# Optimization experiments

Measured on AMD Instinct MI355X. Metric: run time of the kernel, lower is better.

Reference implementation:

```python
import jax, jax.numpy as jnp
import numpy as np

N_NODES = 100000
N_EDGES = 1600000
NFEAT = 512
HIDDEN = 128
NCLASS = 40


def setup_inputs() -> dict:
    key = jax.random.key(0)
    ks = jax.random.split(key, 8)
    x = jax.random.normal(ks[0], (N_NODES, NFEAT), dtype=jnp.float32)
    edge_src = jax.random.randint(ks[1], (N_EDGES,), 0, N_NODES, dtype=jnp.int32)
    edge_dst = jax.random.randint(ks[2], (N_EDGES,), 0, N_NODES, dtype=jnp.int32)
    # normalized adjacency values (D^-1/2 A D^-1/2 style), all positive
    edge_val = jax.random.uniform(ks[3], (N_EDGES,), dtype=jnp.float32)
    # glorot-ish init like pygcn's reset_parameters
    W1 = jax.random.normal(ks[4], (NFEAT, HIDDEN), dtype=jnp.float32) / np.sqrt(NFEAT)
    b1 = jnp.zeros((HIDDEN,), dtype=jnp.float32)
    W2 = jax.random.normal(ks[5], (HIDDEN, NCLASS), dtype=jnp.float32) / np.sqrt(HIDDEN)
    b2 = jnp.zeros((NCLASS,), dtype=jnp.float32)
    return {"x": x, "edge_src": edge_src, "edge_dst": edge_dst, "edge_val": edge_val,
            "W1": W1, "b1": b1, "W2": W2, "b2": b2}


def _gcn_layer(h, edge_src, edge_dst, edge_val, W, b):
    # support = h @ W ; out = spmm(adj, support) + b
    support = h @ W                                  # [N, d_out]
    msg = support[edge_src] * edge_val[:, None]      # [E, d_out] gather
    agg = jax.ops.segment_sum(msg, edge_dst, num_segments=N_NODES)  # scatter-add
    return agg + b


def reference(x, edge_src, edge_dst, edge_val, W1, b1, W2, b2):
    h = _gcn_layer(x, edge_src, edge_dst, edge_val, W1, b1)
    h = jax.nn.relu(h)
    # dropout=0.0 -> branch skipped (faithful to `if self.dropout:` with falsy value)
    h = _gcn_layer(h, edge_src, edge_dst, edge_val, W2, b2)
    return jax.nn.log_softmax(h, axis=1)
```

## Files before the change

kernel.cpp:

```cpp
#include <hip/hip_runtime.h>
#include <stdint.h>

#define NN 100000
#define NE 1600000
#define NF 512
#define NH 128
#define NC 40
#define DEGS 16
#define NGB 782
#define EPB 2048

typedef float f32x4 __attribute__((ext_vector_type(4)));
typedef short bf16x8 __attribute__((ext_vector_type(8)));

__device__ __forceinline__ unsigned short f2bf(float f){
    unsigned u = __float_as_uint(f);
    u = u + 0x7FFFu + ((u >> 16) & 1u);
    return (unsigned short)(u >> 16);
}
__device__ __forceinline__ unsigned pk2(float a, float b){
    return (unsigned)f2bf(a) | ((unsigned)f2bf(b) << 16);
}
__device__ __forceinline__ float blo(unsigned u){ return __uint_as_float(u << 16); }
__device__ __forceinline__ float bhi(unsigned u){ return __uint_as_float(u & 0xffff0000u); }
__device__ __forceinline__ float pval(unsigned p){ return __uint_as_float((p & 0x7fffu) << 16); }
__device__ __forceinline__ unsigned psrc(unsigned p){ return p >> 15; }

__global__ __launch_bounds__(256) void wprep(const float* __restrict__ W1, const float* __restrict__ W2,
                                             unsigned short* __restrict__ W1t, unsigned short* __restrict__ W2t){
    int tid = blockIdx.x * 256 + threadIdx.x;
    if (tid < NF * NH){
        int c = tid >> 9;
        int k = tid & 511;
        W1t[c * NF + k] = f2bf(W1[k * NH + c]);
    }
    int t2 = tid - NF * NH;
    if (t2 >= 0 && t2 < 48 * NH){
        int c = t2 >> 7;
        int k = t2 & 127;
        W2t[c * NH + k] = (c < NC) ? f2bf(W2[k * NC + c]) : (unsigned short)0;
    }
}

__global__ __launch_bounds__(256, 3) void gemm1_edge(const float* __restrict__ x,
                                                     const unsigned short* __restrict__ W1t,
                                                     unsigned short* __restrict__ s1,
                                                     const int* __restrict__ esrc,
                                                     const int* __restrict__ edst,
                                                     const float* __restrict__ eval,
                                                     unsigned* __restrict__ deg,
                                                     unsigned* __restrict__ pkc){
    __shared__ unsigned short Al[2][128 * 40];
    __shared__ unsigned short Bl[2][128 * 40];
    const int tid  = threadIdx.x;

    unsigned epv[8]; unsigned epos[8]; int edd[8];
    {
        const int ebase = blockIdx.x * EPB + tid;
#pragma unroll
        for (int i = 0; i < 8; i++){
            int e = ebase + i * 256;
            bool ok = e < NE;
            int d      = ok ? edst[e] : 0;
            int sv     = ok ? esrc[e] : 0;
            float ev   = ok ? eval[e] : 0.f;
            edd[i] = d;
            epv[i] = ((unsigned)sv << 15) | ((unsigned)f2bf(ev) & 0x7fffu);
            epos[i] = ok ? atomicAdd(&deg[d * DEGS], 1u) : 64u;
        }
    }

    const int wid  = tid >> 6;
    const int lane = tid & 63;
    const int quad = lane >> 4;
    const int l15  = lane & 15;
    const int br   = blockIdx.x * 128;

    const int r    = tid >> 1;
    const int half = tid & 1;

    int arow = br + r; if (arow >= NN) arow = NN - 1;
    const float* aptr = x + (size_t)arow * NF + half * 16;
    const unsigned short* bptr = W1t + (size_t)r * NF + half * 16;

    float4 pa0, pa1, pa2, pa3;
    uint4  pb0, pb1;
    {
        const float4* ap = (const float4*)aptr;
        pa0 = ap[0]; pa1 = ap[1]; pa2 = ap[2]; pa3 = ap[3];
        const uint4* bp = (const uint4*)bptr;
        pb0 = bp[0]; pb1 = bp[1];
        unsigned* Ad = (unsigned*)&Al[0][r * 40 + half * 16];
        Ad[0] = pk2(pa0.x, pa0.y); Ad[1] = pk2(pa0.z, pa0.w);
        Ad[2] = pk2(pa1.x, pa1.y); Ad[3] = pk2(pa1.z, pa1.w);
        Ad[4] = pk2(pa2.x, pa2.y); Ad[5] = pk2(pa2.z, pa2.w);
        Ad[6] = pk2(pa3.x, pa3.y); Ad[7] = pk2(pa3.z, pa3.w);
        uint4* Bd = (uint4*)&Bl[0][r * 40 + half * 16];
        Bd[0] = pb0; Bd[1] = pb1;
    }
    __syncthreads();

    f32x4 acc[2][8];
#pragma unroll
    for (int i = 0; i < 2; i++)
#pragma unroll
        for (int j = 0; j < 8; j++) acc[i][j] = (f32x4){0.f, 0.f, 0.f, 0.f};

    int cur = 0;
    for (int ks = 0; ks < NF; ks += 32){
        const bool more = (ks + 32 < NF);
        if (more){
            const float4* ap = (const float4*)(aptr + ks + 32);
            pa0 = ap[0]; pa1 = ap[1]; pa2 = ap[2]; pa3 = ap[3];
            const uint4* bp = (const uint4*)(bptr + ks + 32);
            pb0 = bp[0]; pb1 = bp[1];
        }

        bf16x8 a0 = *(const bf16x8*)&Al[cur][(wid * 32 +      l15) * 40 + quad * 8];
        bf16x8 a1 = *(const bf16x8*)&Al[cur][(wid * 32 + 16 + l15) * 40 + quad * 8];
        bf16x8 bb[8];
#pragma unroll
        for (int ct = 0; ct < 8; ct++)
            bb[ct] = *(const bf16x8*)&Bl[cur][(ct * 16 + l15) * 40 + quad * 8];
#pragma unroll
        for (int ct = 0; ct < 8; ct++){
            acc[0][ct] = __builtin_amdgcn_mfma_f32_16x16x32_bf16(a0, bb[ct], acc[0][ct], 0, 0, 0);
            acc[1][ct] = __builtin_amdgcn_mfma_f32_16x16x32_bf16(a1, bb[ct], acc[1][ct], 0, 0, 0);
        }

        if (more){
            int nxt = cur ^ 1;
            unsigned* Ad = (unsigned*)&Al[nxt][r * 40 + half * 16];
            Ad[0] = pk2(pa0.x, pa0.y); Ad[1] = pk2(pa0.z, pa0.w);
            Ad[2] = pk2(pa1.x, pa1.y); Ad[3] = pk2(pa1.z, pa1.w);
            Ad[4] = pk2(pa2.x, pa2.y); Ad[5] = pk2(pa2.z, pa2.w);
            Ad[6] = pk2(pa3.x, pa3.y); Ad[7] = pk2(pa3.z, pa3.w);
            uint4* Bd = (uint4*)&Bl[nxt][r * 40 + half * 16];
            Bd[0] = pb0; Bd[1] = pb1;
        }
        __syncthreads();
        cur ^= 1;
    }

#pragma unroll
    for (int rt = 0; rt < 2; rt++)
#pragma unroll
        for (int ct = 0; ct < 8; ct++)
#pragma unroll
            for (int i = 0; i < 4; i++){
                int row = br + wid * 32 + rt * 16 + quad * 4 + i;
                if (row < NN) s1[(size_t)row * NH + ct * 16 + l15] = f2bf(acc[rt][ct][i]);
            }

#pragma unroll
    for (int i = 0; i < 8; i++){
        if (epos[i] < 64u)
            pkc[(size_t)edd[i] * 64 + epos[i]] = epv[i];
    }
}

__global__ __launch_bounds__(256) void agg1g2(const uint4* __restrict__ s1v,
                                              const unsigned* __restrict__ deg,
                                              const unsigned* __restrict__ pkc,
                                              const float* __restrict__ b1,
                                              const unsigned short* __restrict__ W2t,
                                              unsigned short* __restrict__ s2p){
    __shared__ unsigned short Hl[64][136];
    const int tid   = threadIdx.x;
    const int wid   = tid >> 6;
    const int lane  = tid & 63;
    const int quad  = lane >> 4;
    const int hl    = lane & 15;
    const int lbase = quad * 16;
    const int nb    = blockIdx.x * 64;

    const float4* b1v = (const float4*)b1;
    const float4 bA = b1v[2 * hl], bB = b1v[2 * hl + 1];

#pragma unroll
    for (int pass = 0; pass < 4; pass++){
        const int nloc = pass * 16 + wid * 4 + quad;
        const int node = nb + nloc;
        float a[8];
#pragma unroll
        for (int t = 0; t < 8; t++) a[t] = 0.f;

        if (node < NN){
            const unsigned s = (unsigned)node * 64;
            unsigned dgv = deg[node * DEGS]; int dg = (dgv > 64u) ? 64 : (int)dgv;
            const unsigned e = s + dg;

            unsigned rec = 0;
            { int c0 = dg > 16 ? 16 : dg; if (hl < c0) rec = pkc[s + hl]; }
            for (unsigned base = s; base < e; base += 16){
                int cnt = (int)(e - base); if (cnt > 16) cnt = 16;
                unsigned curc = rec;
                unsigned nxb = base + 16;
                if (nxb < e){
                    int cn = (int)(e - nxb); if (cn > 16) cn = 16;
                    rec = 0;
                    if (hl < cn) rec = pkc[nxb + hl];
                }
                int j = 0;
                for (; j + 8 <= cnt; j += 8){
                    unsigned ps[8];
#pragma unroll
                    for (int q = 0; q < 8; q++) ps[q] = __shfl(curc, lbase + j + q, 64);
                    uint4 us[8];
#pragma unroll
                    for (int q = 0; q < 8; q++) us[q] = s1v[(size_t)psrc(ps[q]) * 16 + hl];
#pragma unroll
                    for (int q = 0; q < 8; q++){
                        float v = pval(ps[q]);
                        a[0] += v * blo(us[q].x); a[1] += v * bhi(us[q].x);
                        a[2] += v * blo(us[q].y); a[3] += v * bhi(us[q].y);
                        a[4] += v * blo(us[q].z); a[5] += v * bhi(us[q].z);
                        a[6] += v * blo(us[q].w); a[7] += v * bhi(us[q].w);
                    }
                }
                for (; j < cnt; j++){
                    unsigned p = __shfl(curc, lbase + j, 64);
                    float v = pval(p);
                    uint4 u  = s1v[(size_t)psrc(p) * 16 + hl];
                    a[0] += v * blo(u.x); a[1] += v * bhi(u.x);
                    a[2] += v * blo(u.y); a[3] += v * bhi(u.y);
                    a[4] += v * blo(u.z); a[5] += v * bhi(u.z);
                    a[6] += v * blo(u.w); a[7] += v * bhi(u.w);
                }
            }
            a[0] += bA.x; a[1] += bA.y; a[2] += bA.z; a[3] += bA.w;
            a[4] += bB.x; a[5] += bB.y; a[6] += bB.z; a[7] += bB.w;
#pragma unroll
            for (int t = 0; t < 8; t++) a[t] = fmaxf(a[t], 0.f);
        }
        *(uint4*)&Hl[nloc][hl * 8] = make_uint4(pk2(a[0], a[1]), pk2(a[2], a[3]),
                                                pk2(a[4], a[5]), pk2(a[6], a[7]));
    }
    __syncthreads();

    bf16x8 bf[3][4];
#pragma unroll
    for (int ct = 0; ct < 3; ct++)
#pragma unroll
        for (int ks = 0; ks < 4; ks++)
            bf[ct][ks] = *(const bf16x8*)&W2t[(ct * 16 + hl) * NH + ks * 32 + quad * 8];

    bf16x8 af[4];
#pragma unroll
    for (int ks = 0; ks < 4; ks++)
        af[ks] = *(const bf16x8*)&Hl[wid * 16 + hl][ks * 32 + quad * 8];

    f32x4 acc[3];
#pragma unroll
    for (int ct = 0; ct < 3; ct++) acc[ct] = (f32x4){0.f, 0.f, 0.f, 0.f};
#pragma unroll
    for (int ks = 0; ks < 4; ks++)
#pragma unroll
        for (int ct = 0; ct < 3; ct++)
            acc[ct] = __builtin_amdgcn_mfma_f32_16x16x32_bf16(af[ks], bf[ct][ks], acc[ct], 0, 0, 0);

#pragma unroll
    for (int ct = 0; ct < 3; ct++)
#pragma unroll
        for (int i = 0; i < 4; i++){
            int row = nb + wid * 16 + quad * 4 + i;
            if (row < NN) s2p[(size_t)row * 64 + ct * 16 + hl] = f2bf(acc[ct][i]);
        }
}

__global__ __launch_bounds__(256) void agg2(const uint4* __restrict__ s2v,
                                            const unsigned* __restrict__ deg,
                                            const unsigned* __restrict__ pkc,
                                            const float* __restrict__ b2, float* __restrict__ out){
    const int lane  = threadIdx.x & 63;
    const int oct   = lane >> 3;
    const int hl    = lane & 7;
    const int lbase = oct * 8;
    const int node  = blockIdx.x * 32 + (threadIdx.x >> 6) * 8 + oct;

    float a[8];
#pragma unroll
    for (int t = 0; t < 8; t++) a[t] = 0.f;

    const unsigned s = (unsigned)node * 64;
    unsigned dgv = deg[node * DEGS]; int dg = (dgv > 64u) ? 64 : (int)dgv;
    const unsigned e = s + dg;

    unsigned rec = 0;
    { int c0 = dg > 8 ? 8 : dg; if (hl < c0) rec = pkc[s + hl]; }
    for (unsigned base = s; base < e; base += 8){
        int cnt = (int)(e - base); if (cnt > 8) cnt = 8;
        unsigned curc = rec;
        unsigned nxb = base + 8;
        if (nxb < e){
            int cn = (int)(e - nxb); if (cn > 8) cn = 8;
            rec = 0;
            if (hl < cn) rec = pkc[nxb + hl];
        }
        int j = 0;
        for (; j + 4 <= cnt; j += 4){
            unsigned ps[4];
#pragma unroll
            for (int q = 0; q < 4; q++) ps[q] = __shfl(curc, lbase + j + q, 64);
            uint4 us[4];
#pragma unroll
            for (int q = 0; q < 4; q++) us[q] = s2v[(size_t)psrc(ps[q]) * 8 + hl];
#pragma unroll
            for (int q = 0; q < 4; q++){
                float v = pval(ps[q]);
                a[0] += v * blo(us[q].x); a[1] += v * bhi(us[q].x);
                a[2] += v * blo(us[q].y); a[3] += v * bhi(us[q].y);
                a[4] += v * blo(us[q].z); a[5] += v * bhi(us[q].z);
                a[6] += v * blo(us[q].w); a[7] += v * bhi(us[q].w);
            }
        }
        for (; j < cnt; j++){
            unsigned p = __shfl(curc, lbase + j, 64);
            float v = pval(p);
            uint4 u  = s2v[(size_t)psrc(p) * 8 + hl];
            a[0] += v * blo(u.x); a[1] += v * bhi(u.x);
            a[2] += v * blo(u.y); a[3] += v * bhi(u.y);
            a[4] += v * blo(u.z); a[5] += v * bhi(u.z);
            a[6] += v * blo(u.w); a[7] += v * bhi(u.w);
        }
    }
    const bool act = hl < 5;
    float z[8];
    if (act){
        const float4* b2v = (const float4*)b2;
        float4 cA = b2v[2 * hl], cB = b2v[2 * hl + 1];
        z[0] = a[0] + cA.x; z[1] = a[1] + cA.y; z[2] = a[2] + cA.z; z[3] = a[3] + cA.w;
        z[4] = a[4] + cB.x; z[5] = a[5] + cB.y; z[6] = a[6] + cB.z; z[7] = a[7] + cB.w;
    } else {
#pragma unroll
        for (int t = 0; t < 8; t++) z[t] = -INFINITY;
    }
    float m = z[0];
#pragma unroll
    for (int t = 1; t < 8; t++) m = fmaxf(m, z[t]);
#pragma unroll
    for (int o = 4; o; o >>= 1) m = fmaxf(m, __shfl_xor(m, o, 64));
    float pe = 0.f;
    if (act){
#pragma unroll
        for (int t = 0; t < 8; t++) pe += __expf(z[t] - m);
    }
#pragma unroll
    for (int o = 4; o; o >>= 1) pe += __shfl_xor(pe, o, 64);
    if (act){
        float l = __logf(pe) + m;
        float* op = out + (size_t)node * NC + 8 * hl;
        *(float4*)op       = make_float4(z[0] - l, z[1] - l, z[2] - l, z[3] - l);
        *(float4*)(op + 4) = make_float4(z[4] - l, z[5] - l, z[6] - l, z[7] - l);
    }
}

extern "C" void kernel_launch(void* const* d_in, const int* in_sizes, int n_in,
                              void* d_out, int out_size, void* d_ws, size_t ws_size,
                              hipStream_t stream) {
    const float* x    = (const float*)d_in[0];
    const int*   esrc = (const int*)  d_in[1];
    const int*   edst = (const int*)  d_in[2];
    const float* eval = (const float*)d_in[3];
    const float* W1   = (const float*)d_in[4];
    const float* b1   = (const float*)d_in[5];
    const float* W2   = (const float*)d_in[6];
    const float* b2   = (const float*)d_in[7];
    float* out = (float*)d_out;

    char* ws = (char*)d_ws;
    size_t off = 0;
    auto alloc = [&](size_t bytes) -> void* {
        void* p = ws + off;
        off += (bytes + 255) & ~(size_t)255;
        return p;
    };
    unsigned short* W1t  = (unsigned short*)alloc((size_t)NF * NH * 2);
    unsigned short* W2t  = (unsigned short*)alloc((size_t)48 * NH * 2);
    unsigned short* s1   = (unsigned short*)alloc((size_t)NN * NH * 2);
    unsigned short* s2p  = (unsigned short*)alloc((size_t)NN * 64 * 2);
    unsigned*       deg  = (unsigned*)     alloc((size_t)NN * DEGS * 4);
    unsigned*       pkc  = (unsigned*)     alloc((size_t)NN * 64 * 4);

    hipMemsetAsync(deg, 0, (size_t)NN * DEGS * 4, stream);

    wprep     <<<280, 256, 0, stream>>>(W1, W2, W1t, W2t);
    gemm1_edge<<<NGB, 256, 0, stream>>>(x, W1t, s1, esrc, edst, eval, deg, pkc);
    agg1g2    <<<(NN + 63) / 64, 256, 0, stream>>>((const uint4*)s1, deg, pkc, b1, W2t, s2p);
    agg2      <<<NN / 32, 256, 0, stream>>>((const uint4*)s2p, deg, pkc, b2, out);
}
```

Measured before the change: 533.0 us.

## Split edge bucketing into separate interleaved blocks alongside GEMM blocks

The fused GEMM1-plus-edge-bucketing kernel now launches five times as many blocks. One in five runs the GEMM tile and the other four each handle 512 edges: they do the degree atomic and write the packed entry immediately. This takes the edge work, and the registers that held its state, out of the GEMM blocks, which may raise GEMM occupancy and lets the atomic-heavy scatter spread across more waves. The cost is more blocks, smaller edge chunks per block, and possible contention between the two kinds of block.

```diff
diff --git a/kernel.cpp b/kernel.cpp
--- a/kernel.cpp
+++ b/kernel.cpp
@@ -8,7 +8,8 @@
 #define NC 40
 #define DEGS 16
 #define NGB 782
-#define EPB 2048
+#define STRIPE 5
+#define NEB 3125
 
 typedef float f32x4 __attribute__((ext_vector_type(4)));
 typedef short bf16x8 __attribute__((ext_vector_type(8)));
@@ -52,29 +53,31 @@
                                                      unsigned* __restrict__ pkc){
     __shared__ unsigned short Al[2][128 * 40];
     __shared__ unsigned short Bl[2][128 * 40];
-    const int tid  = threadIdx.x;
-
-    unsigned epv[8]; unsigned epos[8]; int edd[8];
-    {
-        const int ebase = blockIdx.x * EPB + tid;
-#pragma unroll
-        for (int i = 0; i < 8; i++){
-            int e = ebase + i * 256;
-            bool ok = e < NE;
-            int d      = ok ? edst[e] : 0;
-            int sv     = ok ? esrc[e] : 0;
-            float ev   = ok ? eval[e] : 0.f;
-            edd[i] = d;
-            epv[i] = ((unsigned)sv << 15) | ((unsigned)f2bf(ev) & 0x7fffu);
-            epos[i] = ok ? atomicAdd(&deg[d * DEGS], 1u) : 64u;
-        }
+    const int bid = blockIdx.x;
+    const int tid = threadIdx.x;
+
+    if (bid % STRIPE != 0){
+        int ebid = (bid / STRIPE) * 4 + (bid % STRIPE) - 1;
+        int t0 = ebid * 512 + tid;
+#pragma unroll
+        for (int i = 0; i < 2; i++){
+            int e = t0 + i * 256;
+            if (e < NE){
+                int d = edst[e];
+                unsigned pv = ((unsigned)esrc[e] << 15) | ((unsigned)f2bf(eval[e]) & 0x7fffu);
+                unsigned pos = atomicAdd(&deg[d * DEGS], 1u);
+                if (pos < 64u)
+                    pkc[(size_t)d * 64 + pos] = pv;
+            }
+        }
+        return;
     }
 
     const int wid  = tid >> 6;
     const int lane = tid & 63;
     const int quad = lane >> 4;
     const int l15  = lane & 15;
-    const int br   = blockIdx.x * 128;
+    const int br   = (bid / STRIPE) * 128;
 
     const int r    = tid >> 1;
     const int half = tid & 1;
@@ -151,12 +154,6 @@
                 int row = br + wid * 32 + rt * 16 + quad * 4 + i;
                 if (row < NN) s1[(size_t)row * NH + ct * 16 + l15] = f2bf(acc[rt][ct][i]);
             }
-
-#pragma unroll
-    for (int i = 0; i < 8; i++){
-        if (epos[i] < 64u)
-            pkc[(size_t)edd[i] * 64 + epos[i]] = epv[i];
-    }
 }
 
 __global__ __launch_bounds__(256) void agg1g2(const uint4* __restrict__ s1v,
@@ -385,7 +382,7 @@
     hipMemsetAsync(deg, 0, (size_t)NN * DEGS * 4, stream);
 
     wprep     <<<280, 256, 0, stream>>>(W1, W2, W1t, W2t);
-    gemm1_edge<<<NGB, 256, 0, stream>>>(x, W1t, s1, esrc, edst, eval, deg, pkc);
+    gemm1_edge<<<NGB * STRIPE, 256, 0, stream>>>(x, W1t, s1, esrc, edst, eval, deg, pkc);
     agg1g2    <<<(NN + 63) / 64, 256, 0, stream>>>((const uint4*)s1, deg, pkc, b1, W2t, s2p);
     agg2      <<<NN / 32, 256, 0, stream>>>((const uint4*)s2p, deg, pkc, b2, out);
 }
```

New measurement: 489.9 us. 8.1% less time.
